# Kernel tuning notes

Measured on AMD Instinct MI355X. Metric: run time of the kernel, lower is better.

The kernel has to match this reference:

```python
import jax, jax.numpy as jnp
import numpy as np

B, C, H, W = 2, 256, 128, 128
G, S = 2, 4  # group_num, stride


def setup_inputs() -> dict:
    key = jax.random.key(0)
    ks = jax.random.split(key, 6)
    x = jax.random.normal(ks[0], (B, C, H, W), jnp.float32)
    qkv_w = jax.random.normal(ks[1], (C + C // 2, C), jnp.float32) * 0.02
    qkv_b = jax.random.normal(ks[2], (C + C // 2,), jnp.float32) * 0.02
    out_w = jax.random.normal(ks[3], (C, C), jnp.float32) * 0.02
    out_b = jax.random.normal(ks[4], (C,), jnp.float32) * 0.02
    gamma = jax.random.normal(ks[5], (1,), jnp.float32) * 0.1
    return {"x": x, "qkv_w": qkv_w, "qkv_b": qkv_b, "out_w": out_w,
            "out_b": out_b, "gamma": gamma, "mode": 0}


def reference(x, qkv_w, qkv_b, out_w, out_b, gamma, mode):
    b, c, h, w = x.shape
    g, s = G, S
    b1, c1, c2 = b * g, c // 4 // g, c // g
    h1, w1 = h // s, w // s
    n1, n = h1 * w1, h * w
    # 1x1 QKV conv
    qkv = jnp.einsum('oc,bchw->bohw', qkv_w, x) + qkv_b[None, :, None, None]
    Q = qkv[:, :c // 4]
    K = qkv[:, c // 4:c // 2]
    V = qkv[:, c // 2:]
    # avg_pool2d with kernel=stride=s (non-overlapping) via reshape-mean
    pool = lambda t: t.reshape(b, c // 4, h1, s, w1, s).mean(axis=(3, 5))
    q = pool(Q).reshape(b1, c1, n1)
    k = pool(K).reshape(b1, c1, n1)
    Qf = Q.reshape(b1, c1, n)
    Kf = K.reshape(b1, c1, n)
    Vf = V.reshape(b1, c2, n)
    # attention maps; softmax over dim=1 (the row / key index)
    A_c = jax.nn.softmax(jnp.einsum('bki,bkj->bij', k, Qf), axis=1)   # [b1,n1,n]
    A_m = jax.nn.softmax(jnp.einsum('bki,bkj->bij', k, q), axis=1)    # [b1,n1,n1]
    A_s = jax.nn.softmax(jnp.einsum('bki,bkj->bij', Kf, q), axis=1)   # [b1,n,n1]
    e = jnp.eye(n1, dtype=x.dtype)
    # E: each pooled-token identity row expanded over its s x s spatial block
    E = jnp.broadcast_to(e.reshape(n1, h1, 1, w1, 1),
                         (n1, h1, s, w1, s)).reshape(n1, n)
    A_c = jnp.linalg.inv(A_m + e) @ (A_c + E)                          # [b1,n1,n]
    O = (Vf @ A_s) @ A_c                                               # [b1,c2,n]
    out = O.reshape(b, c, h, w)
    out = jnp.einsum('oc,bchw->bohw', out_w, out) + out_b[None, :, None, None]
    if mode == 0:
        out = gamma[0] * out + x
    return out
```

## Files before the change

### kernel.cpp

```cpp
#include <hip/hip_runtime.h>
#include <cstdint>
#include <cstddef>

#define HWN 16384
#define NP1 1024
#define RL2E 1.44269504f

typedef __attribute__((ext_vector_type(8))) short bf16x8;
typedef __attribute__((ext_vector_type(8))) unsigned short ushort8v;
typedef __attribute__((ext_vector_type(4))) unsigned short ushort4v;
typedef __attribute__((ext_vector_type(2))) unsigned int uint2v;
typedef __attribute__((ext_vector_type(4))) unsigned int uint4v;
typedef __attribute__((ext_vector_type(4))) float f32x4;

__device__ __forceinline__ unsigned short f2bu(float f) {
  unsigned int u = __builtin_bit_cast(unsigned int, f);
  u = (u + 0x7FFFu + ((u >> 16) & 1u)) >> 16;
  return (unsigned short)u;
}
__device__ __forceinline__ float b2f(unsigned short s) {
  unsigned int u = ((unsigned int)s) << 16;
  return __builtin_bit_cast(float, u);
}
__device__ __forceinline__ unsigned cvtpk(float lo, float hi) {
  unsigned r;
  asm("v_cvt_pk_bf16_f32 %0, %1, %2" : "=v"(r) : "v"(lo), "v"(hi));
  return r;
}
__device__ __forceinline__ bf16x8 scale_l2e(ushort8v t) {
  ushort8v o;
#pragma unroll
  for (int q = 0; q < 8; ++q) o[q] = f2bu(RL2E * b2f(t[q]));
  return __builtin_bit_cast(bf16x8, o);
}
__device__ __forceinline__ bf16x8 ones_frag() {
  ushort8v o;
#pragma unroll
  for (int q = 0; q < 8; ++q) o[q] = 0x3F80u;
  return __builtin_bit_cast(bf16x8, o);
}
#define MFMA16(A,B,C) __builtin_amdgcn_mfma_f32_16x16x32_bf16((A),(B),(C),0,0,0)
#define PIDX(r,c) ((((r) << 6) + (c)) ^ (((r) & 7) << 3))

__global__ __launch_bounds__(256) void k_cast(
    const float* __restrict__ x, const float* __restrict__ qkv_w,
    const float* __restrict__ out_w, unsigned short* __restrict__ xbT,
    unsigned short* __restrict__ wqb, unsigned short* __restrict__ wob) {
  int bid = blockIdx.x, t = threadIdx.x;
  if (bid < 2048) {
    __shared__ float Lt[64][65];
    int b = bid >> 10, rest = bid & 1023, ct = rest >> 8, pt = rest & 255;
    const float* xp = x + ((size_t)b * 256 + ct * 64) * HWN + pt * 64;
    for (int it = 0; it < 16; ++it) {
      int idx = it * 256 + t; int cc = idx >> 6, pp = idx & 63;
      Lt[cc][pp] = xp[(size_t)cc * HWN + pp];
    }
    __syncthreads();
    int prow = t >> 2, c0 = (t & 3) * 16;
    unsigned short* dst = xbT + ((size_t)b * HWN + pt * 64 + prow) * 256 + ct * 64 + c0;
    uint4v o1, o2;
#pragma unroll
    for (int q = 0; q < 4; ++q) o1[q] = cvtpk(Lt[c0 + 2*q][prow], Lt[c0 + 2*q + 1][prow]);
#pragma unroll
    for (int q = 0; q < 4; ++q) o2[q] = cvtpk(Lt[c0 + 8 + 2*q][prow], Lt[c0 + 9 + 2*q][prow]);
    *(uint4v*)dst = o1;
    *(uint4v*)(dst + 8) = o2;
  } else {
    int base = (bid - 2048) * 1024 + t * 4;
    if (base < 98304) {
      float4 v = *(const float4*)(qkv_w + base);
      uint2v o; o[0] = cvtpk(v.x, v.y); o[1] = cvtpk(v.z, v.w);
      *(uint2v*)(wqb + base) = o;
    } else {
      int b2 = base - 98304;
      float4 v = *(const float4*)(out_w + b2);
      uint2v o; o[0] = cvtpk(v.x, v.y); o[1] = cvtpk(v.z, v.w);
      *(uint2v*)(wob + b2) = o;
    }
  }
}

__global__ __launch_bounds__(256) void k_qkv(
    const unsigned short* __restrict__ wqb, const unsigned short* __restrict__ xbT,
    const float* __restrict__ qkv_b, unsigned short* __restrict__ qkvb,
    unsigned short* __restrict__ kT) {
  int pt = blockIdx.x, b = blockIdx.y;
  int tid = threadIdx.x, w = tid >> 6, lane = tid & 63;
  int lg = lane >> 4, ln = lane & 15;
  f32x4 acc[6][4] = {};
#pragma unroll
  for (int ks = 0; ks < 8; ++ks) {
    int c0 = ks * 32;
    bf16x8 bx[4];
#pragma unroll
    for (int nt = 0; nt < 4; ++nt)
      bx[nt] = *(const bf16x8*)(xbT + ((size_t)b * HWN + pt * 64 + nt * 16 + ln) * 256 + c0 + lg * 8);
#pragma unroll
    for (int ot = 0; ot < 6; ++ot) {
      bf16x8 aw = *(const bf16x8*)(wqb + (size_t)(ot * 64 + w * 16 + ln) * 256 + c0 + lg * 8);
#pragma unroll
      for (int nt = 0; nt < 4; ++nt)
        acc[ot][nt] = MFMA16(aw, bx[nt], acc[ot][nt]);
    }
  }
#pragma unroll
  for (int ot = 0; ot < 6; ++ot) {
    int ob = ot * 64 + w * 16 + lg * 4;
    float b0 = qkv_b[ob], b1 = qkv_b[ob + 1], b2 = qkv_b[ob + 2], b3 = qkv_b[ob + 3];
#pragma unroll
    for (int nt = 0; nt < 4; ++nt) {
      int p = pt * 64 + nt * 16 + ln;
      unsigned u01 = cvtpk(acc[ot][nt][0] + b0, acc[ot][nt][1] + b1);
      unsigned u23 = cvtpk(acc[ot][nt][2] + b2, acc[ot][nt][3] + b3);
      size_t qb = ((size_t)b * 384 + ob) * HWN + p;
      qkvb[qb]           = (unsigned short)u01;
      qkvb[qb + HWN]     = (unsigned short)(u01 >> 16);
      qkvb[qb + 2 * HWN] = (unsigned short)u23;
      qkvb[qb + 3 * HWN] = (unsigned short)(u23 >> 16);
      if (ot == 1) {
        int bgi = b * 2 + (w >> 1);
        int d0 = (w & 1) * 16 + lg * 4;
        uint2v kv; kv[0] = u01; kv[1] = u23;
        *(uint2v*)(kT + ((size_t)bgi * HWN + p) * 32 + d0) = kv;
      }
    }
  }
}

__global__ __launch_bounds__(256) void k_pool(
    const unsigned short* __restrict__ qkvb, unsigned short* __restrict__ qpb,
    unsigned short* __restrict__ kpt) {
  int idx = blockIdx.x * 256 + threadIdx.x;
  int i1 = idx & 1023, cc = (idx >> 10) & 31, bg = idx >> 15;
  int b = bg >> 1, g = bg & 1;
  int h1 = i1 >> 5, w1 = i1 & 31;
  const unsigned short* bq = qkvb + (size_t)(b * 384 + g * 32 + cc) * HWN;
  const unsigned short* bk = qkvb + (size_t)(b * 384 + 64 + g * 32 + cc) * HWN;
  float sq = 0.f, sk = 0.f;
#pragma unroll
  for (int sh = 0; sh < 4; ++sh) {
    int off = (h1 * 4 + sh) * 128 + w1 * 4;
    ushort4v vq = *(const ushort4v*)(bq + off);
    ushort4v vk = *(const ushort4v*)(bk + off);
#pragma unroll
    for (int e = 0; e < 4; ++e) { sq += b2f(vq[e]); sk += b2f(vk[e]); }
  }
  qpb[((size_t)bg * 32 + cc) * NP1 + i1] = f2bu(sq * 0.0625f);
  kpt[((size_t)bg * NP1 + i1) * 32 + cc] = f2bu(sk * 0.0625f);
}

__global__ __launch_bounds__(256) void k_score(
    const unsigned short* __restrict__ qpb, const unsigned short* __restrict__ kpt,
    unsigned short* __restrict__ Eut, float* __restrict__ lpart) {
  int jt = blockIdx.x, ic = blockIdx.y, bg = blockIdx.z;
  int tid = threadIdx.x, w = tid >> 6, lane = tid & 63;
  int lg = lane >> 4, ln = lane & 15;
  __shared__ float redL[4][64];
  bf16x8 bq[4];
#pragma unroll
  for (int nt = 0; nt < 4; ++nt) {
    ushort8v t8;
#pragma unroll
    for (int jr = 0; jr < 8; ++jr)
      t8[jr] = qpb[((size_t)bg * 32 + lg * 8 + jr) * NP1 + jt * 64 + nt * 16 + ln];
    bq[nt] = scale_l2e(t8);
  }
  float lsum[4] = {0.f, 0.f, 0.f, 0.f};
  for (int chk = 0; chk < 4; ++chk) {
    int i0 = ic * 256 + chk * 64;
    bf16x8 ak = *(const bf16x8*)(kpt + ((size_t)bg * NP1 + i0 + w * 16 + ln) * 32 + lg * 8);
#pragma unroll
    for (int nt = 0; nt < 4; ++nt) {
      f32x4 z = {0.f, 0.f, 0.f, 0.f};
      f32x4 s = MFMA16(ak, bq[nt], z);
      float e0 = exp2f(s[0]), e1 = exp2f(s[1]), e2 = exp2f(s[2]), e3 = exp2f(s[3]);
      lsum[nt] += (e0 + e1) + (e2 + e3);
      int j = jt * 64 + nt * 16 + ln;
      int ib = i0 + w * 16 + lg * 4;
      uint2v pk;
      pk[0] = cvtpk(e0, e1);
      pk[1] = cvtpk(e2, e3);
      *(uint2v*)(Eut + ((size_t)bg * NP1 + j) * NP1 + ib) = pk;
    }
  }
#pragma unroll
  for (int nt = 0; nt < 4; ++nt) {
    float v = lsum[nt];
    v += __shfl_xor(v, 16); v += __shfl_xor(v, 32);
    if (lane < 16) redL[w][nt * 16 + lane] = v;
  }
  __syncthreads();
  if (tid < 64)
    lpart[((size_t)(bg * 4 + ic)) * NP1 + jt * 64 + tid] =
        redL[0][tid] + redL[1][tid] + redL[2][tid] + redL[3][tid];
}

__global__ __launch_bounds__(256) void k_rvec2(
    const unsigned short* __restrict__ Eut, const float* __restrict__ lpart,
    float* __restrict__ linv, float* __restrict__ rvecp) {
  int jc = blockIdx.x, bg = blockIdx.y, t = threadIdx.x;
  __shared__ float linv_s[32];
  if (t < 32) {
    int j = jc * 32 + t;
    float l = lpart[((size_t)(bg * 4 + 0)) * NP1 + j] + lpart[((size_t)(bg * 4 + 1)) * NP1 + j] +
              lpart[((size_t)(bg * 4 + 2)) * NP1 + j] + lpart[((size_t)(bg * 4 + 3)) * NP1 + j];
    float inv = 1.f / l;
    linv_s[t] = inv;
    linv[(size_t)bg * NP1 + j] = inv;
  }
  __syncthreads();
  int i0 = t * 4;
  float a0 = 0.f, a1 = 0.f, a2 = 0.f, a3 = 0.f;
#pragma unroll 8
  for (int jj = 0; jj < 32; ++jj) {
    float li = linv_s[jj];
    ushort4v e4 = *(const ushort4v*)(Eut + ((size_t)bg * NP1 + jc * 32 + jj) * NP1 + i0);
    a0 += b2f(e4[0]) * li; a1 += b2f(e4[1]) * li;
    a2 += b2f(e4[2]) * li; a3 += b2f(e4[3]) * li;
  }
  float4 o = {a0, a1, a2, a3};
  *(float4*)(rvecp + ((size_t)(jc * 4 + bg)) * NP1 + i0) = o;
}

__global__ __launch_bounds__(256) void k_flashW1(
    const unsigned short* __restrict__ qkvb, const unsigned short* __restrict__ kT,
    const unsigned short* __restrict__ qpb,
    float* __restrict__ pacc, float* __restrict__ pl) {
  int n = blockIdx.x + (blockIdx.y << 4) + (blockIdx.z << 7);
  int wid = ((n & 7) << 6) + (n >> 3);
  int jt = wid & 15, kc = (wid >> 4) & 7, bg = wid >> 7;
  int b = bg >> 1, g = bg & 1;
  int tid = threadIdx.x, w = tid >> 6, lane = tid & 63;
  int lg = lane >> 4, ln = lane & 15;
  __shared__ unsigned short PtS[2][64 * 64];
  __shared__ float redL[4][64];
  const int Vch = b * 384 + 128 + g * 128;
  bf16x8 bq[4];
#pragma unroll
  for (int nt = 0; nt < 4; ++nt) {
    ushort8v t8;
#pragma unroll
    for (int jr = 0; jr < 8; ++jr)
      t8[jr] = qpb[((size_t)bg * 32 + lg * 8 + jr) * NP1 + jt * 64 + nt * 16 + ln];
    bq[nt] = scale_l2e(t8);
  }
  f32x4 acc[2][4] = {};
  float lsum[4] = {0.f, 0.f, 0.f, 0.f};
  const int i0base = kc * 2048;
  const unsigned short* kTbase = kT + ((size_t)bg * HWN + i0base + w * 16 + ln) * 32 + lg * 8;
  const unsigned short* Vrow0 = qkvb + (size_t)(Vch + w * 32 + ln) * HWN + i0base + lg * 8;
  const unsigned short* Vrow1 = qkvb + (size_t)(Vch + w * 32 + 16 + ln) * HWN + i0base + lg * 8;

  bf16x8 akA, akB;
  bf16x8 avA[4], avB[4];
  akA = *(const bf16x8*)(kTbase);
  {
    f32x4 sn[4];
#pragma unroll
    for (int nt = 0; nt < 4; ++nt) { f32x4 z = {0.f,0.f,0.f,0.f}; sn[nt] = MFMA16(akA, bq[nt], z); }
    akB = *(const bf16x8*)(kTbase + 2048);
    avA[0] = *(const bf16x8*)(Vrow0);
    avA[1] = *(const bf16x8*)(Vrow1);
    avA[2] = *(const bf16x8*)(Vrow0 + 32);
    avA[3] = *(const bf16x8*)(Vrow1 + 32);
#pragma unroll
    for (int nt = 0; nt < 4; ++nt) {
      float e0 = exp2f(sn[nt][0]), e1 = exp2f(sn[nt][1]), e2 = exp2f(sn[nt][2]), e3 = exp2f(sn[nt][3]);
      lsum[nt] += (e0 + e1) + (e2 + e3);
      uint2v pk; pk[0] = cvtpk(e0, e1); pk[1] = cvtpk(e2, e3);
      *(uint2v*)&PtS[0][PIDX(nt * 16 + ln, w * 16 + lg * 4)] = pk;
    }
  }
  for (int pr = 0; pr < 16; ++pr) {
    int c = pr * 2;
    __syncthreads();
    f32x4 sn[4];
#pragma unroll
    for (int nt = 0; nt < 4; ++nt) { f32x4 z = {0.f,0.f,0.f,0.f}; sn[nt] = MFMA16(akB, bq[nt], z); }
    {
      int c2 = (c + 2) & 31, c1 = c + 1;
      akA = *(const bf16x8*)(kTbase + (size_t)c2 * 2048);
      avB[0] = *(const bf16x8*)(Vrow0 + c1 * 64);
      avB[1] = *(const bf16x8*)(Vrow1 + c1 * 64);
      avB[2] = *(const bf16x8*)(Vrow0 + c1 * 64 + 32);
      avB[3] = *(const bf16x8*)(Vrow1 + c1 * 64 + 32);
    }
    __builtin_amdgcn_s_setprio(1);
#pragma unroll
    for (int ist = 0; ist < 2; ++ist) {
      bf16x8 bp[4];
#pragma unroll
      for (int nt = 0; nt < 4; ++nt)
        bp[nt] = *(const bf16x8*)&PtS[0][PIDX(nt * 16 + ln, ist * 32 + lg * 8)];
#pragma unroll
      for (int nt = 0; nt < 4; ++nt) {
        acc[0][nt] = MFMA16(avA[ist * 2 + 0], bp[nt], acc[0][nt]);
        acc[1][nt] = MFMA16(avA[ist * 2 + 1], bp[nt], acc[1][nt]);
      }
    }
    __builtin_amdgcn_s_setprio(0);
#pragma unroll
    for (int nt = 0; nt < 4; ++nt) {
      float e0 = exp2f(sn[nt][0]), e1 = exp2f(sn[nt][1]), e2 = exp2f(sn[nt][2]), e3 = exp2f(sn[nt][3]);
      lsum[nt] += (e0 + e1) + (e2 + e3);
      uint2v pk; pk[0] = cvtpk(e0, e1); pk[1] = cvtpk(e2, e3);
      *(uint2v*)&PtS[1][PIDX(nt * 16 + ln, w * 16 + lg * 4)] = pk;
    }
    __syncthreads();
    if (pr < 15) {
#pragma unroll
      for (int nt = 0; nt < 4; ++nt) { f32x4 z = {0.f,0.f,0.f,0.f}; sn[nt] = MFMA16(akA, bq[nt], z); }
      int c3 = c + 3, c2 = c + 2;
      akB = *(const bf16x8*)(kTbase + (size_t)c3 * 2048);
      avA[0] = *(const bf16x8*)(Vrow0 + c2 * 64);
      avA[1] = *(const bf16x8*)(Vrow1 + c2 * 64);
      avA[2] = *(const bf16x8*)(Vrow0 + c2 * 64 + 32);
      avA[3] = *(const bf16x8*)(Vrow1 + c2 * 64 + 32);
    }
    __builtin_amdgcn_s_setprio(1);
#pragma unroll
    for (int ist = 0; ist < 2; ++ist) {
      bf16x8 bp[4];
#pragma unroll
      for (int nt = 0; nt < 4; ++nt)
        bp[nt] = *(const bf16x8*)&PtS[1][PIDX(nt * 16 + ln, ist * 32 + lg * 8)];
#pragma unroll
      for (int nt = 0; nt < 4; ++nt) {
        acc[0][nt] = MFMA16(avB[ist * 2 + 0], bp[nt], acc[0][nt]);
        acc[1][nt] = MFMA16(avB[ist * 2 + 1], bp[nt], acc[1][nt]);
      }
    }
    __builtin_amdgcn_s_setprio(0);
    if (pr < 15) {
#pragma unroll
      for (int nt = 0; nt < 4; ++nt) {
        float e0 = exp2f(sn[nt][0]), e1 = exp2f(sn[nt][1]), e2 = exp2f(sn[nt][2]), e3 = exp2f(sn[nt][3]);
        lsum[nt] += (e0 + e1) + (e2 + e3);
        uint2v pk; pk[0] = cvtpk(e0, e1); pk[1] = cvtpk(e2, e3);
        *(uint2v*)&PtS[0][PIDX(nt * 16 + ln, w * 16 + lg * 4)] = pk;
      }
    }
  }
  size_t pb = (((size_t)bg * 16 + jt) * 8 + kc) * 8192;
#pragma unroll
  for (int ct = 0; ct < 2; ++ct)
#pragma unroll
    for (int nt = 0; nt < 4; ++nt)
#pragma unroll
      for (int r = 0; r < 4; ++r)
        pacc[pb + (size_t)(w * 32 + ct * 16 + lg * 4 + r) * 64 + nt * 16 + ln] = acc[ct][nt][r];
#pragma unroll
  for (int nt = 0; nt < 4; ++nt) {
    float v = lsum[nt];
    v += __shfl_xor(v, 16); v += __shfl_xor(v, 32);
    if (lane < 16) redL[w][nt * 16 + lane] = v;
  }
  __syncthreads();
  if (tid < 64)
    pl[(((size_t)bg * 16 + jt) * 8 + kc) * 64 + tid] =
        redL[0][tid] + redL[1][tid] + redL[2][tid] + redL[3][tid];
}

__global__ __launch_bounds__(256) void k_combine(
    const float* __restrict__ pacc, const float* __restrict__ pl,
    float* __restrict__ Yf) {
  int gid = blockIdx.x * 256 + threadIdx.x;
  int bg = gid >> 17, rem = gid & 131071;
  int c = rem >> 10, j = rem & 1023;
  int jt = j >> 6, jj = j & 63;
  float s = 0.f, l = 0.f;
#pragma unroll
  for (int kc = 0; kc < 8; ++kc) {
    size_t pb = ((size_t)bg * 16 + jt) * 8 + kc;
    s += pacc[pb * 8192 + c * 64 + jj];
    l += pl[pb * 64 + jj];
  }
  Yf[gid] = s / l;
}

__global__ __launch_bounds__(256) void k_proj(
    const float* __restrict__ rvecp, float* __restrict__ Yf,
    unsigned short* __restrict__ U0b) {
  int ct = blockIdx.x, bg = blockIdx.y, t = threadIdx.x;
  __shared__ float rs[1024];
  __shared__ float red[256];
  __shared__ float crow[8];
  __shared__ float sSs;
  for (int j = t; j < 1024; j += 256) {
    float s = 0.f;
#pragma unroll
    for (int p = 0; p < 32; ++p) s += rvecp[((size_t)(p * 4 + bg)) * NP1 + j];
    rs[j] = s;
  }
  __syncthreads();
  float p = rs[t] + rs[t + 256] + rs[t + 512] + rs[t + 768];
  red[t] = p; __syncthreads();
  for (int s = 128; s > 0; s >>= 1) {
    if (t < s) red[t] += red[t + s];
    __syncthreads();
  }
  if (t == 0) sSs = red[0];
  __syncthreads();
  int row = t >> 5, ln32 = t & 31;
  const float* yrow = Yf + ((size_t)(bg * 128 + ct * 8 + row)) * NP1;
  float a = 0.f;
  for (int j = ln32; j < 1024; j += 32) a += yrow[j] * rs[j];
#pragma unroll
  for (int m = 1; m <= 16; m <<= 1) a += __shfl_xor(a, m, 32);
  if (ln32 == 0) crow[row] = a / sSs;
  __syncthreads();
  for (int e = t; e < 8 * 1024; e += 256) {
    int rr = e >> 10, j = e & 1023;
    size_t o = ((size_t)(bg * 128 + ct * 8 + rr)) * NP1 + j;
    float y = Yf[o], cv = crow[rr];
    Yf[o] = y - 0.5f * cv;
    U0b[o] = f2bu(y - cv);
  }
}

__global__ __launch_bounds__(256) void k_neu(
    const unsigned short* __restrict__ Vin, const unsigned short* __restrict__ Eut,
    const float* __restrict__ linv, float* __restrict__ W2f,
    unsigned short* __restrict__ Vout, unsigned short* __restrict__ W2b,
    float sgn, int last) {
  int jt = blockIdx.x, ct = blockIdx.y, bg = blockIdx.z;
  int tid = threadIdx.x, w = tid >> 6, lane = tid & 63;
  int lg = lane >> 4, ln = lane & 15;
  int j0 = jt * 32, c0 = ct * 64 + w * 16;
  f32x4 acc[2] = {};
  for (int ks = 0; ks < 32; ++ks) {
    int i0 = ks * 32;
    bf16x8 a = *(const bf16x8*)(Vin + ((size_t)(bg * 128) + c0 + ln) * NP1 + i0 + lg * 8);
#pragma unroll
    for (int nt = 0; nt < 2; ++nt) {
      bf16x8 bt = *(const bf16x8*)(Eut + ((size_t)bg * NP1 + j0 + nt * 16 + ln) * NP1 + i0 + lg * 8);
      acc[nt] = MFMA16(a, bt, acc[nt]);
    }
  }
#pragma unroll
  for (int nt = 0; nt < 2; ++nt) {
    int j = j0 + nt * 16 + ln;
    float li = linv[(size_t)bg * NP1 + j];
#pragma unroll
    for (int r = 0; r < 4; ++r) {
      size_t o = ((size_t)(bg * 128) + c0 + lg * 4 + r) * NP1 + j;
      float v = acc[nt][r] * li;
      if (last) W2b[o] = f2bu(W2f[o] + sgn * v);
      else { Vout[o] = f2bu(v); W2f[o] += sgn * v; }
    }
  }
}

__global__ __launch_bounds__(256) void k_flashO(
    const unsigned short* __restrict__ qkvb, const unsigned short* __restrict__ kpt,
    const unsigned short* __restrict__ W2b, unsigned short* __restrict__ Ot) {
  int jt = blockIdx.x, bg = blockIdx.y;
  int b = bg >> 1, g = bg & 1;
  int tid = threadIdx.x, w = tid >> 6, lane = tid & 63;
  int lg = lane >> 4, ln = lane & 15;
  __shared__ unsigned short PtS[2][64 * 64];
  const int Qch = b * 384 + g * 32;
  bf16x8 aone = ones_frag();
  bf16x8 bq[4];
#pragma unroll
  for (int nt = 0; nt < 4; ++nt) {
    ushort8v t8;
#pragma unroll
    for (int jr = 0; jr < 8; ++jr)
      t8[jr] = qkvb[(size_t)(Qch + lg * 8 + jr) * HWN + jt * 64 + nt * 16 + ln];
    bq[nt] = scale_l2e(t8);
  }
  f32x4 acc[2][4] = {};
  f32x4 asum[4] = {};
  const unsigned short* kbase = kpt + ((size_t)bg * NP1 + w * 16 + ln) * 32 + lg * 8;
  const unsigned short* Wrow0 = W2b + ((size_t)bg * 128 + w * 32 + ln) * NP1 + lg * 8;
  const unsigned short* Wrow1 = W2b + ((size_t)bg * 128 + w * 32 + 16 + ln) * NP1 + lg * 8;

  bf16x8 akA, akB;
  bf16x8 avA[4], avB[4];
  akA = *(const bf16x8*)(kbase);
  {
    f32x4 sn[4];
#pragma unroll
    for (int nt = 0; nt < 4; ++nt) { f32x4 z = {0.f,0.f,0.f,0.f}; sn[nt] = MFMA16(akA, bq[nt], z); }
    akB = *(const bf16x8*)(kbase + 2048);
    avA[0] = *(const bf16x8*)(Wrow0);
    avA[1] = *(const bf16x8*)(Wrow1);
    avA[2] = *(const bf16x8*)(Wrow0 + 32);
    avA[3] = *(const bf16x8*)(Wrow1 + 32);
#pragma unroll
    for (int nt = 0; nt < 4; ++nt) {
      uint2v pk;
      pk[0] = cvtpk(exp2f(sn[nt][0]), exp2f(sn[nt][1]));
      pk[1] = cvtpk(exp2f(sn[nt][2]), exp2f(sn[nt][3]));
      *(uint2v*)&PtS[0][PIDX(nt * 16 + ln, w * 16 + lg * 4)] = pk;
    }
  }
  for (int pr = 0; pr < 8; ++pr) {
    int c = pr * 2;
    __syncthreads();
    f32x4 sn[4];
#pragma unroll
    for (int nt = 0; nt < 4; ++nt) { f32x4 z = {0.f,0.f,0.f,0.f}; sn[nt] = MFMA16(akB, bq[nt], z); }
    {
      int c2 = (c + 2) & 15, c1 = c + 1;
      akA = *(const bf16x8*)(kbase + (size_t)c2 * 2048);
      avB[0] = *(const bf16x8*)(Wrow0 + c1 * 64);
      avB[1] = *(const bf16x8*)(Wrow1 + c1 * 64);
      avB[2] = *(const bf16x8*)(Wrow0 + c1 * 64 + 32);
      avB[3] = *(const bf16x8*)(Wrow1 + c1 * 64 + 32);
    }
    __builtin_amdgcn_s_setprio(1);
#pragma unroll
    for (int ist = 0; ist < 2; ++ist) {
      bf16x8 bp[4];
#pragma unroll
      for (int nt = 0; nt < 4; ++nt)
        bp[nt] = *(const bf16x8*)&PtS[0][PIDX(nt * 16 + ln, ist * 32 + lg * 8)];
#pragma unroll
      for (int nt = 0; nt < 4; ++nt) {
        acc[0][nt] = MFMA16(avA[ist * 2 + 0], bp[nt], acc[0][nt]);
        acc[1][nt] = MFMA16(avA[ist * 2 + 1], bp[nt], acc[1][nt]);
      }
#pragma unroll
      for (int nt = 0; nt < 4; ++nt)
        asum[nt] = MFMA16(aone, bp[nt], asum[nt]);
    }
    __builtin_amdgcn_s_setprio(0);
#pragma unroll
    for (int nt = 0; nt < 4; ++nt) {
      uint2v pk;
      pk[0] = cvtpk(exp2f(sn[nt][0]), exp2f(sn[nt][1]));
      pk[1] = cvtpk(exp2f(sn[nt][2]), exp2f(sn[nt][3]));
      *(uint2v*)&PtS[1][PIDX(nt * 16 + ln, w * 16 + lg * 4)] = pk;
    }
    __syncthreads();
    if (pr < 7) {
#pragma unroll
      for (int nt = 0; nt < 4; ++nt) { f32x4 z = {0.f,0.f,0.f,0.f}; sn[nt] = MFMA16(akA, bq[nt], z); }
      int c3 = c + 3, c2 = c + 2;
      akB = *(const bf16x8*)(kbase + (size_t)c3 * 2048);
      avA[0] = *(const bf16x8*)(Wrow0 + c2 * 64);
      avA[1] = *(const bf16x8*)(Wrow1 + c2 * 64);
      avA[2] = *(const bf16x8*)(Wrow0 + c2 * 64 + 32);
      avA[3] = *(const bf16x8*)(Wrow1 + c2 * 64 + 32);
    }
    __builtin_amdgcn_s_setprio(1);
#pragma unroll
    for (int ist = 0; ist < 2; ++ist) {
      bf16x8 bp[4];
#pragma unroll
      for (int nt = 0; nt < 4; ++nt)
        bp[nt] = *(const bf16x8*)&PtS[1][PIDX(nt * 16 + ln, ist * 32 + lg * 8)];
#pragma unroll
      for (int nt = 0; nt < 4; ++nt) {
        acc[0][nt] = MFMA16(avB[ist * 2 + 0], bp[nt], acc[0][nt]);
        acc[1][nt] = MFMA16(avB[ist * 2 + 1], bp[nt], acc[1][nt]);
      }
#pragma unroll
      for (int nt = 0; nt < 4; ++nt)
        asum[nt] = MFMA16(aone, bp[nt], asum[nt]);
    }
    __builtin_amdgcn_s_setprio(0);
    if (pr < 7) {
#pragma unroll
      for (int nt = 0; nt < 4; ++nt) {
        uint2v pk;
        pk[0] = cvtpk(exp2f(sn[nt][0]), exp2f(sn[nt][1]));
        pk[1] = cvtpk(exp2f(sn[nt][2]), exp2f(sn[nt][3]));
        *(uint2v*)&PtS[0][PIDX(nt * 16 + ln, w * 16 + lg * 4)] = pk;
      }
    }
  }
#pragma unroll
  for (int nt = 0; nt < 4; ++nt) {
    int jj = nt * 16 + ln;
    int jg = jt * 64 + jj;
    float li = 1.f / asum[nt][0];
    int i1 = (jg >> 9) * 32 + ((jg & 127) >> 2);
#pragma unroll
    for (int ct = 0; ct < 2; ++ct) {
      int c = w * 32 + ct * 16 + lg * 4;
      float v0 = acc[ct][nt][0] * li + b2f(W2b[((size_t)bg * 128 + c + 0) * NP1 + i1]);
      float v1 = acc[ct][nt][1] * li + b2f(W2b[((size_t)bg * 128 + c + 1) * NP1 + i1]);
      float v2 = acc[ct][nt][2] * li + b2f(W2b[((size_t)bg * 128 + c + 2) * NP1 + i1]);
      float v3 = acc[ct][nt][3] * li + b2f(W2b[((size_t)bg * 128 + c + 3) * NP1 + i1]);
      uint2v o2; o2[0] = cvtpk(v0, v1); o2[1] = cvtpk(v2, v3);
      *(uint2v*)(Ot + ((size_t)b * HWN + jg) * 256 + g * 128 + c) = o2;
    }
  }
}

__global__ __launch_bounds__(256) void k_out(
    const unsigned short* __restrict__ wob, const unsigned short* __restrict__ Ot,
    const float* __restrict__ out_b, const unsigned short* __restrict__ xbT,
    const float* __restrict__ gamma, const int* __restrict__ mode,
    float* __restrict__ out) {
  int pt = blockIdx.x, b = blockIdx.y;
  int tid = threadIdx.x, w = tid >> 6, lane = tid & 63;
  int lg = lane >> 4, ln = lane & 15;
  f32x4 acc[4][4] = {};
#pragma unroll
  for (int ks = 0; ks < 8; ++ks) {
    int c0 = ks * 32;
    bf16x8 bx[4];
#pragma unroll
    for (int nt = 0; nt < 4; ++nt)
      bx[nt] = *(const bf16x8*)(Ot + ((size_t)b * HWN + pt * 64 + nt * 16 + ln) * 256 + c0 + lg * 8);
#pragma unroll
    for (int h = 0; h < 4; ++h) {
      bf16x8 aw = *(const bf16x8*)(wob + (size_t)(h * 64 + w * 16 + ln) * 256 + c0 + lg * 8);
#pragma unroll
      for (int nt = 0; nt < 4; ++nt)
        acc[h][nt] = MFMA16(aw, bx[nt], acc[h][nt]);
    }
  }
  float gm = gamma[0];
  int md = mode[0];
#pragma unroll
  for (int h = 0; h < 4; ++h) {
    int o0 = h * 64 + w * 16 + lg * 4;
    float b0 = out_b[o0], b1 = out_b[o0 + 1], b2 = out_b[o0 + 2], b3 = out_b[o0 + 3];
#pragma unroll
    for (int nt = 0; nt < 4; ++nt) {
      int p = pt * 64 + nt * 16 + ln;
      ushort4v xr = *(const ushort4v*)(xbT + ((size_t)b * HWN + p) * 256 + o0);
      float v0 = acc[h][nt][0] + b0, v1 = acc[h][nt][1] + b1;
      float v2 = acc[h][nt][2] + b2, v3 = acc[h][nt][3] + b3;
      size_t off = ((size_t)b * 256 + o0) * HWN + p;
      if (md == 0) {
        out[off]           = gm * v0 + b2f(xr[0]);
        out[off + HWN]     = gm * v1 + b2f(xr[1]);
        out[off + 2 * HWN] = gm * v2 + b2f(xr[2]);
        out[off + 3 * HWN] = gm * v3 + b2f(xr[3]);
      } else {
        out[off]           = v0;
        out[off + HWN]     = v1;
        out[off + 2 * HWN] = v2;
        out[off + 3 * HWN] = v3;
      }
    }
  }
}

extern "C" void kernel_launch(void* const* d_in, const int* in_sizes, int n_in,
                              void* d_out, int out_size, void* d_ws, size_t ws_size,
                              hipStream_t stream) {
  (void)in_sizes; (void)n_in; (void)out_size;
  const float* x     = (const float*)d_in[0];
  const float* qkv_w = (const float*)d_in[1];
  const float* qkv_b = (const float*)d_in[2];
  const float* out_w = (const float*)d_in[3];
  const float* out_b = (const float*)d_in[4];
  const float* gamma = (const float*)d_in[5];
  const int*   mode  = (const int*)d_in[6];
  float* out = (float*)d_out;

  char* wsb = (char*)d_ws;
  size_t off = 0;
  auto alloc = [&](size_t bytes) { char* p = wsb + off; off += bytes; return p; };
  unsigned short* xbT  = (unsigned short*)alloc(16777216);
  unsigned short* wqb  = (unsigned short*)alloc(196608);
  unsigned short* wob  = (unsigned short*)alloc(131072);
  unsigned short* qkvb = (unsigned short*)alloc(25165824);
  unsigned short* kT   = (unsigned short*)alloc(4194304);
  unsigned short* qpb  = (unsigned short*)alloc(262144);
  unsigned short* kpt  = (unsigned short*)alloc(262144);
  unsigned short* Eut  = (unsigned short*)alloc(8388608);
  float*          lpart= (float*)alloc(65536);
  float*          linv = (float*)alloc(16384);
  float*          rvecp= (float*)alloc(524288);
  float*          pacc = (float*)alloc(16777216);
  float*          pl   = (float*)alloc(131072);
  float*          Yf   = (float*)alloc(2097152);
  unsigned short* U0b  = (unsigned short*)alloc(1048576);
  unsigned short* Va   = (unsigned short*)alloc(1048576);
  unsigned short* Vb   = (unsigned short*)alloc(1048576);
  unsigned short* W2b  = (unsigned short*)alloc(1048576);
  unsigned short* Ot   = (unsigned short*)pacc;
  (void)Vb;
  if (ws_size < off) return;

  k_cast<<<2208, 256, 0, stream>>>(x, qkv_w, out_w, xbT, wqb, wob);
  k_qkv<<<dim3(256, 2), 256, 0, stream>>>(wqb, xbT, qkv_b, qkvb, kT);
  k_pool<<<512, 256, 0, stream>>>(qkvb, qpb, kpt);
  k_score<<<dim3(16, 4, 4), 256, 0, stream>>>(qpb, kpt, Eut, lpart);
  k_rvec2<<<dim3(32, 4), 256, 0, stream>>>(Eut, lpart, linv, rvecp);
  k_flashW1<<<dim3(16, 8, 4), 256, 0, stream>>>(qkvb, kT, qpb, pacc, pl);
  k_combine<<<2048, 256, 0, stream>>>(pacc, pl, Yf);
  k_proj<<<dim3(16, 4), 256, 0, stream>>>(rvecp, Yf, U0b);
  k_neu<<<dim3(32, 2, 4), 256, 0, stream>>>(U0b, Eut, linv, Yf, Va, W2b, -1.f, 0);
  k_neu<<<dim3(32, 2, 4), 256, 0, stream>>>(Va,  Eut, linv, Yf, Vb, W2b, +1.f, 1);
  k_flashO<<<dim3(256, 4), 256, 0, stream>>>(qkvb, kpt, W2b, Ot);
  k_out<<<dim3(256, 2), 256, 0, stream>>>(wob, Ot, out_b, xbT, gamma, mode, out);
}
```

Baseline: 209.7 us.

## Merge independent score and flash kernels into combined launches; use VALU row sums

Folds the independent pooled-score kernel into the flashW1 launch as extra blocks, and the rvec kernel into the combine launch, which cuts the launch count from four to two and lets the small kernels fill idle CUs next to the large ones. In k_flashO, the row sums are now accumulated from the fp32 exponentials with shuffles and a shared-memory reduction, replacing the extra MFMA against a ones fragment. This drops MFMA work but adds a block reduction and barriers. Block-level branching may also raise register pressure in the fused kernels.

New measurement: 203.1 us. 3.1% less time.

```diff
diff --git a/kernel.cpp b/kernel.cpp
--- a/kernel.cpp
+++ b/kernel.cpp
@@ -31,12 +31,6 @@
   ushort8v o;
 #pragma unroll
   for (int q = 0; q < 8; ++q) o[q] = f2bu(RL2E * b2f(t[q]));
-  return __builtin_bit_cast(bf16x8, o);
-}
-__device__ __forceinline__ bf16x8 ones_frag() {
-  ushort8v o;
-#pragma unroll
-  for (int q = 0; q < 8; ++q) o[q] = 0x3F80u;
   return __builtin_bit_cast(bf16x8, o);
 }
 #define MFMA16(A,B,C) __builtin_amdgcn_mfma_f32_16x16x32_bf16((A),(B),(C),0,0,0)
@@ -149,189 +143,50 @@
   kpt[((size_t)bg * NP1 + i1) * 32 + cc] = f2bu(sk * 0.0625f);
 }
 
-__global__ __launch_bounds__(256) void k_score(
+__global__ __launch_bounds__(256) void k_fw1s(
+    const unsigned short* __restrict__ qkvb, const unsigned short* __restrict__ kT,
     const unsigned short* __restrict__ qpb, const unsigned short* __restrict__ kpt,
+    float* __restrict__ pacc, float* __restrict__ pl,
     unsigned short* __restrict__ Eut, float* __restrict__ lpart) {
-  int jt = blockIdx.x, ic = blockIdx.y, bg = blockIdx.z;
+  __shared__ unsigned short PtS[2][64 * 64];
+  __shared__ float redL[4][64];
+  int n = blockIdx.x;
   int tid = threadIdx.x, w = tid >> 6, lane = tid & 63;
   int lg = lane >> 4, ln = lane & 15;
-  __shared__ float redL[4][64];
-  bf16x8 bq[4];
-#pragma unroll
-  for (int nt = 0; nt < 4; ++nt) {
-    ushort8v t8;
-#pragma unroll
-    for (int jr = 0; jr < 8; ++jr)
-      t8[jr] = qpb[((size_t)bg * 32 + lg * 8 + jr) * NP1 + jt * 64 + nt * 16 + ln];
-    bq[nt] = scale_l2e(t8);
-  }
-  float lsum[4] = {0.f, 0.f, 0.f, 0.f};
-  for (int chk = 0; chk < 4; ++chk) {
-    int i0 = ic * 256 + chk * 64;
-    bf16x8 ak = *(const bf16x8*)(kpt + ((size_t)bg * NP1 + i0 + w * 16 + ln) * 32 + lg * 8);
-#pragma unroll
-    for (int nt = 0; nt < 4; ++nt) {
-      f32x4 z = {0.f, 0.f, 0.f, 0.f};
-      f32x4 s = MFMA16(ak, bq[nt], z);
-      float e0 = exp2f(s[0]), e1 = exp2f(s[1]), e2 = exp2f(s[2]), e3 = exp2f(s[3]);
-      lsum[nt] += (e0 + e1) + (e2 + e3);
-      int j = jt * 64 + nt * 16 + ln;
-      int ib = i0 + w * 16 + lg * 4;
-      uint2v pk;
-      pk[0] = cvtpk(e0, e1);
-      pk[1] = cvtpk(e2, e3);
-      *(uint2v*)(Eut + ((size_t)bg * NP1 + j) * NP1 + ib) = pk;
-    }
-  }
-#pragma unroll
-  for (int nt = 0; nt < 4; ++nt) {
-    float v = lsum[nt];
-    v += __shfl_xor(v, 16); v += __shfl_xor(v, 32);
-    if (lane < 16) redL[w][nt * 16 + lane] = v;
-  }
-  __syncthreads();
-  if (tid < 64)
-    lpart[((size_t)(bg * 4 + ic)) * NP1 + jt * 64 + tid] =
-        redL[0][tid] + redL[1][tid] + redL[2][tid] + redL[3][tid];
-}
-
-__global__ __launch_bounds__(256) void k_rvec2(
-    const unsigned short* __restrict__ Eut, const float* __restrict__ lpart,
-    float* __restrict__ linv, float* __restrict__ rvecp) {
-  int jc = blockIdx.x, bg = blockIdx.y, t = threadIdx.x;
-  __shared__ float linv_s[32];
-  if (t < 32) {
-    int j = jc * 32 + t;
-    float l = lpart[((size_t)(bg * 4 + 0)) * NP1 + j] + lpart[((size_t)(bg * 4 + 1)) * NP1 + j] +
-              lpart[((size_t)(bg * 4 + 2)) * NP1 + j] + lpart[((size_t)(bg * 4 + 3)) * NP1 + j];
-    float inv = 1.f / l;
-    linv_s[t] = inv;
-    linv[(size_t)bg * NP1 + j] = inv;
-  }
-  __syncthreads();
-  int i0 = t * 4;
-  float a0 = 0.f, a1 = 0.f, a2 = 0.f, a3 = 0.f;
-#pragma unroll 8
-  for (int jj = 0; jj < 32; ++jj) {
-    float li = linv_s[jj];
-    ushort4v e4 = *(const ushort4v*)(Eut + ((size_t)bg * NP1 + jc * 32 + jj) * NP1 + i0);
-    a0 += b2f(e4[0]) * li; a1 += b2f(e4[1]) * li;
-    a2 += b2f(e4[2]) * li; a3 += b2f(e4[3]) * li;
-  }
-  float4 o = {a0, a1, a2, a3};
-  *(float4*)(rvecp + ((size_t)(jc * 4 + bg)) * NP1 + i0) = o;
-}
-
-__global__ __launch_bounds__(256) void k_flashW1(
-    const unsigned short* __restrict__ qkvb, const unsigned short* __restrict__ kT,
-    const unsigned short* __restrict__ qpb,
-    float* __restrict__ pacc, float* __restrict__ pl) {
-  int n = blockIdx.x + (blockIdx.y << 4) + (blockIdx.z << 7);
-  int wid = ((n & 7) << 6) + (n >> 3);
-  int jt = wid & 15, kc = (wid >> 4) & 7, bg = wid >> 7;
-  int b = bg >> 1, g = bg & 1;
-  int tid = threadIdx.x, w = tid >> 6, lane = tid & 63;
-  int lg = lane >> 4, ln = lane & 15;
-  __shared__ unsigned short PtS[2][64 * 64];
-  __shared__ float redL[4][64];
-  const int Vch = b * 384 + 128 + g * 128;
-  bf16x8 bq[4];
-#pragma unroll
-  for (int nt = 0; nt < 4; ++nt) {
-    ushort8v t8;
-#pragma unroll
-    for (int jr = 0; jr < 8; ++jr)
-      t8[jr] = qpb[((size_t)bg * 32 + lg * 8 + jr) * NP1 + jt * 64 + nt * 16 + ln];
-    bq[nt] = scale_l2e(t8);
-  }
-  f32x4 acc[2][4] = {};
-  float lsum[4] = {0.f, 0.f, 0.f, 0.f};
-  const int i0base = kc * 2048;
-  const unsigned short* kTbase = kT + ((size_t)bg * HWN + i0base + w * 16 + ln) * 32 + lg * 8;
-  const unsigned short* Vrow0 = qkvb + (size_t)(Vch + w * 32 + ln) * HWN + i0base + lg * 8;
-  const unsigned short* Vrow1 = qkvb + (size_t)(Vch + w * 32 + 16 + ln) * HWN + i0base + lg * 8;
-
-  bf16x8 akA, akB;
-  bf16x8 avA[4], avB[4];
-  akA = *(const bf16x8*)(kTbase);
-  {
-    f32x4 sn[4];
-#pragma unroll
-    for (int nt = 0; nt < 4; ++nt) { f32x4 z = {0.f,0.f,0.f,0.f}; sn[nt] = MFMA16(akA, bq[nt], z); }
-    akB = *(const bf16x8*)(kTbase + 2048);
-    avA[0] = *(const bf16x8*)(Vrow0);
-    avA[1] = *(const bf16x8*)(Vrow1);
-    avA[2] = *(const bf16x8*)(Vrow0 + 32);
-    avA[3] = *(const bf16x8*)(Vrow1 + 32);
-#pragma unroll
-    for (int nt = 0; nt < 4; ++nt) {
-      float e0 = exp2f(sn[nt][0]), e1 = exp2f(sn[nt][1]), e2 = exp2f(sn[nt][2]), e3 = exp2f(sn[nt][3]);
-      lsum[nt] += (e0 + e1) + (e2 + e3);
-      uint2v pk; pk[0] = cvtpk(e0, e1); pk[1] = cvtpk(e2, e3);
-      *(uint2v*)&PtS[0][PIDX(nt * 16 + ln, w * 16 + lg * 4)] = pk;
-    }
-  }
-  for (int pr = 0; pr < 16; ++pr) {
-    int c = pr * 2;
-    __syncthreads();
-    f32x4 sn[4];
-#pragma unroll
-    for (int nt = 0; nt < 4; ++nt) { f32x4 z = {0.f,0.f,0.f,0.f}; sn[nt] = MFMA16(akB, bq[nt], z); }
+
+  if (n < 512) {
+    int wid = ((n & 7) << 6) + (n >> 3);
+    int jt = wid & 15, kc = (wid >> 4) & 7, bg = wid >> 7;
+    int b = bg >> 1, g = bg & 1;
+    const int Vch = b * 384 + 128 + g * 128;
+    bf16x8 bq[4];
+#pragma unroll
+    for (int nt = 0; nt < 4; ++nt) {
+      ushort8v t8;
+#pragma unroll
+      for (int jr = 0; jr < 8; ++jr)
+        t8[jr] = qpb[((size_t)bg * 32 + lg * 8 + jr) * NP1 + jt * 64 + nt * 16 + ln];
+      bq[nt] = scale_l2e(t8);
+    }
+    f32x4 acc[2][4] = {};
+    float lsum[4] = {0.f, 0.f, 0.f, 0.f};
+    const int i0base = kc * 2048;
+    const unsigned short* kTbase = kT + ((size_t)bg * HWN + i0base + w * 16 + ln) * 32 + lg * 8;
+    const unsigned short* Vrow0 = qkvb + (size_t)(Vch + w * 32 + ln) * HWN + i0base + lg * 8;
+    const unsigned short* Vrow1 = qkvb + (size_t)(Vch + w * 32 + 16 + ln) * HWN + i0base + lg * 8;
+
+    bf16x8 akA, akB;
+    bf16x8 avA[4], avB[4];
+    akA = *(const bf16x8*)(kTbase);
     {
-      int c2 = (c + 2) & 31, c1 = c + 1;
-      akA = *(const bf16x8*)(kTbase + (size_t)c2 * 2048);
-      avB[0] = *(const bf16x8*)(Vrow0 + c1 * 64);
-      avB[1] = *(const bf16x8*)(Vrow1 + c1 * 64);
-      avB[2] = *(const bf16x8*)(Vrow0 + c1 * 64 + 32);
-      avB[3] = *(const bf16x8*)(Vrow1 + c1 * 64 + 32);
-    }
-    __builtin_amdgcn_s_setprio(1);
-#pragma unroll
-    for (int ist = 0; ist < 2; ++ist) {
-      bf16x8 bp[4];
-#pragma unroll
-      for (int nt = 0; nt < 4; ++nt)
-        bp[nt] = *(const bf16x8*)&PtS[0][PIDX(nt * 16 + ln, ist * 32 + lg * 8)];
-#pragma unroll
-      for (int nt = 0; nt < 4; ++nt) {
-        acc[0][nt] = MFMA16(avA[ist * 2 + 0], bp[nt], acc[0][nt]);
-        acc[1][nt] = MFMA16(avA[ist * 2 + 1], bp[nt], acc[1][nt]);
-      }
-    }
-    __builtin_amdgcn_s_setprio(0);
-#pragma unroll
-    for (int nt = 0; nt < 4; ++nt) {
-      float e0 = exp2f(sn[nt][0]), e1 = exp2f(sn[nt][1]), e2 = exp2f(sn[nt][2]), e3 = exp2f(sn[nt][3]);
-      lsum[nt] += (e0 + e1) + (e2 + e3);
-      uint2v pk; pk[0] = cvtpk(e0, e1); pk[1] = cvtpk(e2, e3);
-      *(uint2v*)&PtS[1][PIDX(nt * 16 + ln, w * 16 + lg * 4)] = pk;
-    }
-    __syncthreads();
-    if (pr < 15) {
+      f32x4 sn[4];
 #pragma unroll
       for (int nt = 0; nt < 4; ++nt) { f32x4 z = {0.f,0.f,0.f,0.f}; sn[nt] = MFMA16(akA, bq[nt], z); }
-      int c3 = c + 3, c2 = c + 2;
-      akB = *(const bf16x8*)(kTbase + (size_t)c3 * 2048);
-      avA[0] = *(const bf16x8*)(Vrow0 + c2 * 64);
-      avA[1] = *(const bf16x8*)(Vrow1 + c2 * 64);
-      avA[2] = *(const bf16x8*)(Vrow0 + c2 * 64 + 32);
-      avA[3] = *(const bf16x8*)(Vrow1 + c2 * 64 + 32);
-    }
-    __builtin_amdgcn_s_setprio(1);
-#pragma unroll
-    for (int ist = 0; ist < 2; ++ist) {
-      bf16x8 bp[4];
-#pragma unroll
-      for (int nt = 0; nt < 4; ++nt)
-        bp[nt] = *(const bf16x8*)&PtS[1][PIDX(nt * 16 + ln, ist * 32 + lg * 8)];
-#pragma unroll
-      for (int nt = 0; nt < 4; ++nt) {
-        acc[0][nt] = MFMA16(avB[ist * 2 + 0], bp[nt], acc[0][nt]);
-        acc[1][nt] = MFMA16(avB[ist * 2 + 1], bp[nt], acc[1][nt]);
-      }
-    }
-    __builtin_amdgcn_s_setprio(0);
-    if (pr < 15) {
+      akB = *(const bf16x8*)(kTbase + 2048);
+      avA[0] = *(const bf16x8*)(Vrow0);
+      avA[1] = *(const bf16x8*)(Vrow1);
+      avA[2] = *(const bf16x8*)(Vrow0 + 32);
+      avA[3] = *(const bf16x8*)(Vrow1 + 32);
 #pragma unroll
       for (int nt = 0; nt < 4; ++nt) {
         float e0 = exp2f(sn[nt][0]), e1 = exp2f(sn[nt][1]), e2 = exp2f(sn[nt][2]), e3 = exp2f(sn[nt][3]);
@@ -340,42 +195,181 @@
         *(uint2v*)&PtS[0][PIDX(nt * 16 + ln, w * 16 + lg * 4)] = pk;
       }
     }
-  }
-  size_t pb = (((size_t)bg * 16 + jt) * 8 + kc) * 8192;
-#pragma unroll
-  for (int ct = 0; ct < 2; ++ct)
-#pragma unroll
-    for (int nt = 0; nt < 4; ++nt)
-#pragma unroll
-      for (int r = 0; r < 4; ++r)
-        pacc[pb + (size_t)(w * 32 + ct * 16 + lg * 4 + r) * 64 + nt * 16 + ln] = acc[ct][nt][r];
-#pragma unroll
-  for (int nt = 0; nt < 4; ++nt) {
-    float v = lsum[nt];
-    v += __shfl_xor(v, 16); v += __shfl_xor(v, 32);
-    if (lane < 16) redL[w][nt * 16 + lane] = v;
-  }
-  __syncthreads();
-  if (tid < 64)
-    pl[(((size_t)bg * 16 + jt) * 8 + kc) * 64 + tid] =
-        redL[0][tid] + redL[1][tid] + redL[2][tid] + redL[3][tid];
-}
-
-__global__ __launch_bounds__(256) void k_combine(
+    for (int pr = 0; pr < 16; ++pr) {
+      int c = pr * 2;
+      __syncthreads();
+      f32x4 sn[4];
+#pragma unroll
+      for (int nt = 0; nt < 4; ++nt) { f32x4 z = {0.f,0.f,0.f,0.f}; sn[nt] = MFMA16(akB, bq[nt], z); }
+      {
+        int c2 = (c + 2) & 31, c1 = c + 1;
+        akA = *(const bf16x8*)(kTbase + (size_t)c2 * 2048);
+        avB[0] = *(const bf16x8*)(Vrow0 + c1 * 64);
+        avB[1] = *(const bf16x8*)(Vrow1 + c1 * 64);
+        avB[2] = *(const bf16x8*)(Vrow0 + c1 * 64 + 32);
+        avB[3] = *(const bf16x8*)(Vrow1 + c1 * 64 + 32);
+      }
+      __builtin_amdgcn_s_setprio(1);
+#pragma unroll
+      for (int ist = 0; ist < 2; ++ist) {
+        bf16x8 bp[4];
+#pragma unroll
+        for (int nt = 0; nt < 4; ++nt)
+          bp[nt] = *(const bf16x8*)&PtS[0][PIDX(nt * 16 + ln, ist * 32 + lg * 8)];
+#pragma unroll
+        for (int nt = 0; nt < 4; ++nt) {
+          acc[0][nt] = MFMA16(avA[ist * 2 + 0], bp[nt], acc[0][nt]);
+          acc[1][nt] = MFMA16(avA[ist * 2 + 1], bp[nt], acc[1][nt]);
+        }
+      }
+      __builtin_amdgcn_s_setprio(0);
+#pragma unroll
+      for (int nt = 0; nt < 4; ++nt) {
+        float e0 = exp2f(sn[nt][0]), e1 = exp2f(sn[nt][1]), e2 = exp2f(sn[nt][2]), e3 = exp2f(sn[nt][3]);
+        lsum[nt] += (e0 + e1) + (e2 + e3);
+        uint2v pk; pk[0] = cvtpk(e0, e1); pk[1] = cvtpk(e2, e3);
+        *(uint2v*)&PtS[1][PIDX(nt * 16 + ln, w * 16 + lg * 4)] = pk;
+      }
+      __syncthreads();
+      if (pr < 15) {
+#pragma unroll
+        for (int nt = 0; nt < 4; ++nt) { f32x4 z = {0.f,0.f,0.f,0.f}; sn[nt] = MFMA16(akA, bq[nt], z); }
+        int c3 = c + 3, c2 = c + 2;
+        akB = *(const bf16x8*)(kTbase + (size_t)c3 * 2048);
+        avA[0] = *(const bf16x8*)(Vrow0 + c2 * 64);
+        avA[1] = *(const bf16x8*)(Vrow1 + c2 * 64);
+        avA[2] = *(const bf16x8*)(Vrow0 + c2 * 64 + 32);
+        avA[3] = *(const bf16x8*)(Vrow1 + c2 * 64 + 32);
+      }
+      __builtin_amdgcn_s_setprio(1);
+#pragma unroll
+      for (int ist = 0; ist < 2; ++ist) {
+        bf16x8 bp[4];
+#pragma unroll
+        for (int nt = 0; nt < 4; ++nt)
+          bp[nt] = *(const bf16x8*)&PtS[1][PIDX(nt * 16 + ln, ist * 32 + lg * 8)];
+#pragma unroll
+        for (int nt = 0; nt < 4; ++nt) {
+          acc[0][nt] = MFMA16(avB[ist * 2 + 0], bp[nt], acc[0][nt]);
+          acc[1][nt] = MFMA16(avB[ist * 2 + 1], bp[nt], acc[1][nt]);
+        }
+      }
+      __builtin_amdgcn_s_setprio(0);
+      if (pr < 15) {
+#pragma unroll
+        for (int nt = 0; nt < 4; ++nt) {
+          float e0 = exp2f(sn[nt][0]), e1 = exp2f(sn[nt][1]), e2 = exp2f(sn[nt][2]), e3 = exp2f(sn[nt][3]);
+          lsum[nt] += (e0 + e1) + (e2 + e3);
+          uint2v pk; pk[0] = cvtpk(e0, e1); pk[1] = cvtpk(e2, e3);
+          *(uint2v*)&PtS[0][PIDX(nt * 16 + ln, w * 16 + lg * 4)] = pk;
+        }
+      }
+    }
+    size_t pb = (((size_t)bg * 16 + jt) * 8 + kc) * 8192;
+#pragma unroll
+    for (int ct = 0; ct < 2; ++ct)
+#pragma unroll
+      for (int nt = 0; nt < 4; ++nt)
+#pragma unroll
+        for (int r = 0; r < 4; ++r)
+          pacc[pb + (size_t)(w * 32 + ct * 16 + lg * 4 + r) * 64 + nt * 16 + ln] = acc[ct][nt][r];
+#pragma unroll
+    for (int nt = 0; nt < 4; ++nt) {
+      float v = lsum[nt];
+      v += __shfl_xor(v, 16); v += __shfl_xor(v, 32);
+      if (lane < 16) redL[w][nt * 16 + lane] = v;
+    }
+    __syncthreads();
+    if (tid < 64)
+      pl[(((size_t)bg * 16 + jt) * 8 + kc) * 64 + tid] =
+          redL[0][tid] + redL[1][tid] + redL[2][tid] + redL[3][tid];
+  } else {
+    int n2 = n - 512;
+    int jt = n2 & 15, ic = (n2 >> 4) & 3, bg = n2 >> 6;
+    bf16x8 bq[4];
+#pragma unroll
+    for (int nt = 0; nt < 4; ++nt) {
+      ushort8v t8;
+#pragma unroll
+      for (int jr = 0; jr < 8; ++jr)
+        t8[jr] = qpb[((size_t)bg * 32 + lg * 8 + jr) * NP1 + jt * 64 + nt * 16 + ln];
+      bq[nt] = scale_l2e(t8);
+    }
+    float lsum[4] = {0.f, 0.f, 0.f, 0.f};
+    for (int chk = 0; chk < 4; ++chk) {
+      int i0 = ic * 256 + chk * 64;
+      bf16x8 ak = *(const bf16x8*)(kpt + ((size_t)bg * NP1 + i0 + w * 16 + ln) * 32 + lg * 8);
+#pragma unroll
+      for (int nt = 0; nt < 4; ++nt) {
+        f32x4 z = {0.f, 0.f, 0.f, 0.f};
+        f32x4 s = MFMA16(ak, bq[nt], z);
+        float e0 = exp2f(s[0]), e1 = exp2f(s[1]), e2 = exp2f(s[2]), e3 = exp2f(s[3]);
+        lsum[nt] += (e0 + e1) + (e2 + e3);
+        int j = jt * 64 + nt * 16 + ln;
+        int ib = i0 + w * 16 + lg * 4;
+        uint2v pk;
+        pk[0] = cvtpk(e0, e1);
+        pk[1] = cvtpk(e2, e3);
+        *(uint2v*)(Eut + ((size_t)bg * NP1 + j) * NP1 + ib) = pk;
+      }
+    }
+#pragma unroll
+    for (int nt = 0; nt < 4; ++nt) {
+      float v = lsum[nt];
+      v += __shfl_xor(v, 16); v += __shfl_xor(v, 32);
+      if (lane < 16) redL[w][nt * 16 + lane] = v;
+    }
+    __syncthreads();
+    if (tid < 64)
+      lpart[((size_t)(bg * 4 + ic)) * NP1 + jt * 64 + tid] =
+          redL[0][tid] + redL[1][tid] + redL[2][tid] + redL[3][tid];
+  }
+}
+
+__global__ __launch_bounds__(256) void k_comb2(
     const float* __restrict__ pacc, const float* __restrict__ pl,
-    float* __restrict__ Yf) {
-  int gid = blockIdx.x * 256 + threadIdx.x;
-  int bg = gid >> 17, rem = gid & 131071;
-  int c = rem >> 10, j = rem & 1023;
-  int jt = j >> 6, jj = j & 63;
-  float s = 0.f, l = 0.f;
-#pragma unroll
-  for (int kc = 0; kc < 8; ++kc) {
-    size_t pb = ((size_t)bg * 16 + jt) * 8 + kc;
-    s += pacc[pb * 8192 + c * 64 + jj];
-    l += pl[pb * 64 + jj];
-  }
-  Yf[gid] = s / l;
+    float* __restrict__ Yf, const unsigned short* __restrict__ Eut,
+    const float* __restrict__ lpart, float* __restrict__ linv,
+    float* __restrict__ rvecp) {
+  int n = blockIdx.x, t = threadIdx.x;
+  if (n < 2048) {
+    int gid = n * 256 + t;
+    int bg = gid >> 17, rem = gid & 131071;
+    int c = rem >> 10, j = rem & 1023;
+    int jt = j >> 6, jj = j & 63;
+    float s = 0.f, l = 0.f;
+#pragma unroll
+    for (int kc = 0; kc < 8; ++kc) {
+      size_t pb = ((size_t)bg * 16 + jt) * 8 + kc;
+      s += pacc[pb * 8192 + c * 64 + jj];
+      l += pl[pb * 64 + jj];
+    }
+    Yf[gid] = s / l;
+  } else {
+    __shared__ float linv_s[32];
+    int n2 = n - 2048;
+    int jc = n2 & 31, bg = n2 >> 5;
+    if (t < 32) {
+      int j = jc * 32 + t;
+      float l = lpart[((size_t)(bg * 4 + 0)) * NP1 + j] + lpart[((size_t)(bg * 4 + 1)) * NP1 + j] +
+                lpart[((size_t)(bg * 4 + 2)) * NP1 + j] + lpart[((size_t)(bg * 4 + 3)) * NP1 + j];
+      float inv = 1.f / l;
+      linv_s[t] = inv;
+      linv[(size_t)bg * NP1 + j] = inv;
+    }
+    __syncthreads();
+    int i0 = t * 4;
+    float a0 = 0.f, a1 = 0.f, a2 = 0.f, a3 = 0.f;
+#pragma unroll 8
+    for (int jj = 0; jj < 32; ++jj) {
+      float li = linv_s[jj];
+      ushort4v e4 = *(const ushort4v*)(Eut + ((size_t)bg * NP1 + jc * 32 + jj) * NP1 + i0);
+      a0 += b2f(e4[0]) * li; a1 += b2f(e4[1]) * li;
+      a2 += b2f(e4[2]) * li; a3 += b2f(e4[3]) * li;
+    }
+    float4 o = {a0, a1, a2, a3};
+    *(float4*)(rvecp + ((size_t)(jc * 4 + bg)) * NP1 + i0) = o;
+  }
 }
 
 __global__ __launch_bounds__(256) void k_proj(
@@ -459,8 +453,9 @@
   int tid = threadIdx.x, w = tid >> 6, lane = tid & 63;
   int lg = lane >> 4, ln = lane & 15;
   __shared__ unsigned short PtS[2][64 * 64];
+  __shared__ float redL[4][64];
+  __shared__ float smL[64];
   const int Qch = b * 384 + g * 32;
-  bf16x8 aone = ones_frag();
   bf16x8 bq[4];
 #pragma unroll
   for (int nt = 0; nt < 4; ++nt) {
@@ -471,7 +466,7 @@
     bq[nt] = scale_l2e(t8);
   }
   f32x4 acc[2][4] = {};
-  f32x4 asum[4] = {};
+  float lsum[4] = {0.f, 0.f, 0.f, 0.f};
   const unsigned short* kbase = kpt + ((size_t)bg * NP1 + w * 16 + ln) * 32 + lg * 8;
   const unsigned short* Wrow0 = W2b + ((size_t)bg * 128 + w * 32 + ln) * NP1 + lg * 8;
   const unsigned short* Wrow1 = W2b + ((size_t)bg * 128 + w * 32 + 16 + ln) * NP1 + lg * 8;
@@ -490,9 +485,9 @@
     avA[3] = *(const bf16x8*)(Wrow1 + 32);
 #pragma unroll
     for (int nt = 0; nt < 4; ++nt) {
-      uint2v pk;
-      pk[0] = cvtpk(exp2f(sn[nt][0]), exp2f(sn[nt][1]));
-      pk[1] = cvtpk(exp2f(sn[nt][2]), exp2f(sn[nt][3]));
+      float e0 = exp2f(sn[nt][0]), e1 = exp2f(sn[nt][1]), e2 = exp2f(sn[nt][2]), e3 = exp2f(sn[nt][3]);
+      lsum[nt] += (e0 + e1) + (e2 + e3);
+      uint2v pk; pk[0] = cvtpk(e0, e1); pk[1] = cvtpk(e2, e3);
       *(uint2v*)&PtS[0][PIDX(nt * 16 + ln, w * 16 + lg * 4)] = pk;
     }
   }
@@ -522,16 +517,13 @@
         acc[0][nt] = MFMA16(avA[ist * 2 + 0], bp[nt], acc[0][nt]);
         acc[1][nt] = MFMA16(avA[ist * 2 + 1], bp[nt], acc[1][nt]);
       }
-#pragma unroll
-      for (int nt = 0; nt < 4; ++nt)
-        asum[nt] = MFMA16(aone, bp[nt], asum[nt]);
     }
     __builtin_amdgcn_s_setprio(0);
 #pragma unroll
     for (int nt = 0; nt < 4; ++nt) {
-      uint2v pk;
-      pk[0] = cvtpk(exp2f(sn[nt][0]), exp2f(sn[nt][1]));
-      pk[1] = cvtpk(exp2f(sn[nt][2]), exp2f(sn[nt][3]));
+      float e0 = exp2f(sn[nt][0]), e1 = exp2f(sn[nt][1]), e2 = exp2f(sn[nt][2]), e3 = exp2f(sn[nt][3]);
+      lsum[nt] += (e0 + e1) + (e2 + e3);
+      uint2v pk; pk[0] = cvtpk(e0, e1); pk[1] = cvtpk(e2, e3);
       *(uint2v*)&PtS[1][PIDX(nt * 16 + ln, w * 16 + lg * 4)] = pk;
     }
     __syncthreads();
@@ -557,26 +549,32 @@
         acc[0][nt] = MFMA16(avB[ist * 2 + 0], bp[nt], acc[0][nt]);
         acc[1][nt] = MFMA16(avB[ist * 2 + 1], bp[nt], acc[1][nt]);
       }
-#pragma unroll
-      for (int nt = 0; nt < 4; ++nt)
-        asum[nt] = MFMA16(aone, bp[nt], asum[nt]);
     }
     __builtin_amdgcn_s_setprio(0);
     if (pr < 7) {
 #pragma unroll
       for (int nt = 0; nt < 4; ++nt) {
-        uint2v pk;
-        pk[0] = cvtpk(exp2f(sn[nt][0]), exp2f(sn[nt][1]));
-        pk[1] = cvtpk(exp2f(sn[nt][2]), exp2f(sn[nt][3]));
+        float e0 = exp2f(sn[nt][0]), e1 = exp2f(sn[nt][1]), e2 = exp2f(sn[nt][2]), e3 = exp2f(sn[nt][3]);
+        lsum[nt] += (e0 + e1) + (e2 + e3);
+        uint2v pk; pk[0] = cvtpk(e0, e1); pk[1] = cvtpk(e2, e3);
         *(uint2v*)&PtS[0][PIDX(nt * 16 + ln, w * 16 + lg * 4)] = pk;
       }
     }
   }
+#pragma unroll
+  for (int nt = 0; nt < 4; ++nt) {
+    float v = lsum[nt];
+    v += __shfl_xor(v, 16); v += __shfl_xor(v, 32);
+    if (lane < 16) redL[w][nt * 16 + lane] = v;
+  }
+  __syncthreads();
+  if (tid < 64) smL[tid] = redL[0][tid] + redL[1][tid] + redL[2][tid] + redL[3][tid];
+  __syncthreads();
 #pragma unroll
   for (int nt = 0; nt < 4; ++nt) {
     int jj = nt * 16 + ln;
     int jg = jt * 64 + jj;
-    float li = 1.f / asum[nt][0];
+    float li = 1.f / smL[jj];
     int i1 = (jg >> 9) * 32 + ((jg & 127) >> 2);
 #pragma unroll
     for (int ct = 0; ct < 2; ++ct) {
@@ -684,10 +682,8 @@
   k_cast<<<2208, 256, 0, stream>>>(x, qkv_w, out_w, xbT, wqb, wob);
   k_qkv<<<dim3(256, 2), 256, 0, stream>>>(wqb, xbT, qkv_b, qkvb, kT);
   k_pool<<<512, 256, 0, stream>>>(qkvb, qpb, kpt);
-  k_score<<<dim3(16, 4, 4), 256, 0, stream>>>(qpb, kpt, Eut, lpart);
-  k_rvec2<<<dim3(32, 4), 256, 0, stream>>>(Eut, lpart, linv, rvecp);
-  k_flashW1<<<dim3(16, 8, 4), 256, 0, stream>>>(qkvb, kT, qpb, pacc, pl);
-  k_combine<<<2048, 256, 0, stream>>>(pacc, pl, Yf);
+  k_fw1s<<<768, 256, 0, stream>>>(qkvb, kT, qpb, kpt, pacc, pl, Eut, lpart);
+  k_comb2<<<2176, 256, 0, stream>>>(pacc, pl, Yf, Eut, lpart, linv, rvecp);
   k_proj<<<dim3(16, 4), 256, 0, stream>>>(rvecp, Yf, U0b);
   k_neu<<<dim3(32, 2, 4), 256, 0, stream>>>(U0b, Eut, linv, Yf, Va, W2b, -1.f, 0);
   k_neu<<<dim3(32, 2, 4), 256, 0, stream>>>(Va,  Eut, linv, Yf, Vb, W2b, +1.f, 1);
```
